# Optimization experiments

Measured on AMD Instinct MI355X. Metric: run time of the kernel, lower is better.

The kernel has to match this reference:

```python
import jax, jax.numpy as jnp
import numpy as np

N0, N1, N2 = 200000, 100000, 50000
DEG = 16
E0, E1 = N1 * DEG, N2 * DEG
EP = 500000
IN, H, EDGE_IN, MLP_H, NCLS = 64, 128, 16, 128, 8
EPS = 1e-5  # BatchNorm eps


def setup_inputs() -> dict:
    key = jax.random.key(0)
    ks = jax.random.split(key, 22)
    def w(k, shape, fan_in):
        return jax.random.normal(k, shape, dtype=jnp.float32) * (1.0 / np.sqrt(fan_in))
    inp = {
        'x_nodes': jax.random.normal(ks[0], (N0, IN), dtype=jnp.float32),
        'src0': jax.random.randint(ks[1], (E0,), 0, N0, dtype=jnp.int32),
        'dst0': jax.random.randint(ks[2], (E0,), 0, N1, dtype=jnp.int32),
        'src1': jax.random.randint(ks[3], (E1,), 0, N1, dtype=jnp.int32),
        'dst1': jax.random.randint(ks[4], (E1,), 0, N2, dtype=jnp.int32),
        'u': jax.random.randint(ks[5], (EP,), 0, N2, dtype=jnp.int32),
        'v': jax.random.randint(ks[6], (EP,), 0, N2, dtype=jnp.int32),
        'e_feat': jax.random.normal(ks[7], (EP, EDGE_IN), dtype=jnp.float32),
        # SAGEConv layer 0 (DGL mean aggregator: fc_self(h_dst) + fc_neigh(mean_neigh) + bias)
        'Ws0': w(ks[8], (IN, H), IN), 'Wn0': w(ks[9], (IN, H), IN), 'b0': jnp.zeros((H,), jnp.float32),
        'g0': jnp.ones((H,), jnp.float32), 'be0': jnp.zeros((H,), jnp.float32),
        # SAGEConv layer 1
        'Ws1': w(ks[10], (H, H), H), 'Wn1': w(ks[11], (H, H), H), 'b1': jnp.zeros((H,), jnp.float32),
        'g1': jnp.ones((H,), jnp.float32), 'be1': jnp.zeros((H,), jnp.float32),
        # edge MLP: Linear(2H+edge_in, MLP_H) -> ReLU -> (Dropout eval=no-op) -> Linear(MLP_H, NCLS)
        'W1': w(ks[12], (2 * H + EDGE_IN, MLP_H), 2 * H + EDGE_IN), 'bm1': jnp.zeros((MLP_H,), jnp.float32),
        'W2': w(ks[13], (MLP_H, NCLS), MLP_H), 'bm2': jnp.zeros((NCLS,), jnp.float32),
    }
    return inp


def _sage_mean(h_src, src, dst, num_dst, Ws, Wn, b):
    # gather neighbor feats, segment-mean over dst, then linear combine
    msgs = h_src[src]                                            # [E, d]
    agg = jax.ops.segment_sum(msgs, dst, num_segments=num_dst)   # [num_dst, d]
    deg = jax.ops.segment_sum(jnp.ones((src.shape[0],), h_src.dtype), dst, num_segments=num_dst)
    mean = agg / jnp.maximum(deg, 1.0)[:, None]
    h_dst = h_src[:num_dst]
    return h_dst @ Ws + mean @ Wn + b


def _bn_relu(x, gamma, beta):
    # training-mode BatchNorm1d over rows, followed by ReLU
    mu = x.mean(axis=0)
    var = x.var(axis=0)
    return jax.nn.relu(gamma * (x - mu) * jax.lax.rsqrt(var + EPS) + beta)


def reference(x_nodes, src0, dst0, src1, dst1, u, v, e_feat,
              Ws0, Wn0, b0, g0, be0, Ws1, Wn1, b1, g1, be1, W1, bm1, W2, bm2):
    h = _bn_relu(_sage_mean(x_nodes, src0, dst0, N1, Ws0, Wn0, b0), g0, be0)  # [N1, H]
    h = _bn_relu(_sage_mean(h, src1, dst1, N2, Ws1, Wn1, b1), g1, be1)        # [N2, H]
    e_repr = jnp.concatenate([h[u], h[v], e_feat], axis=1)                    # [EP, 2H+edge_in]
    hidden = jax.nn.relu(e_repr @ W1 + bm1)
    return hidden @ W2 + bm2                                                  # [EP, NCLS]
```

## Files before the change

### kernel.cpp

```cpp
#include <hip/hip_runtime.h>
#include <hip/hip_bf16.h>

#define CN0 200000
#define CN1 100000
#define CN2 50000
#define CE0 1600000
#define CE1 800000
#define CEP 500000
#define CIN 64
#define CH  128
#define CEIN 16
#define CMH 128
#define CNCLS 8

typedef __bf16 bf16x8 __attribute__((ext_vector_type(8)));
typedef float  f32x4  __attribute__((ext_vector_type(4)));
typedef unsigned short u16x8 __attribute__((ext_vector_type(8)));
typedef unsigned short u16x4 __attribute__((ext_vector_type(4)));

__device__ inline float b2f(unsigned short u) {
  union { unsigned int i; float f; } x; x.i = ((unsigned int)u) << 16; return x.f;
}
__device__ inline unsigned short f2bu(float f) {
  __hip_bfloat16 h = __float2bfloat16(f);
  return *reinterpret_cast<unsigned short*>(&h);
}

__global__ void k_hist(const int* __restrict__ dst, int n, int* __restrict__ cnt) {
  int i = blockIdx.x * blockDim.x + threadIdx.x;
  if (i < n) atomicAdd(&cnt[dst[i]], 1);
}

__global__ __launch_bounds__(256) void k_scan1(const int* __restrict__ cnt, int n,
                                               int* __restrict__ excl, int* __restrict__ bsum) {
  __shared__ int sh[256];
  int t = threadIdx.x;
  int base = blockIdx.x * 1024 + t * 4;
  int v[4];
#pragma unroll
  for (int i = 0; i < 4; i++) v[i] = (base + i < n) ? cnt[base + i] : 0;
  int tsum = v[0] + v[1] + v[2] + v[3];
  sh[t] = tsum; __syncthreads();
  for (int ofs = 1; ofs < 256; ofs <<= 1) {
    int x = (t >= ofs) ? sh[t - ofs] : 0; __syncthreads();
    sh[t] += x; __syncthreads();
  }
  int run = sh[t] - tsum;
  if (t == 255) bsum[blockIdx.x] = sh[255];
#pragma unroll
  for (int i = 0; i < 4; i++) {
    if (base + i < n) excl[base + i] = run;
    run += v[i];
  }
}

__global__ __launch_bounds__(256) void k_scan2(int* __restrict__ bsum, int n) {
  __shared__ int sh[256];
  int t = threadIdx.x;
  int v = (t < n) ? bsum[t] : 0;
  sh[t] = v; __syncthreads();
  for (int ofs = 1; ofs < 256; ofs <<= 1) {
    int x = (t >= ofs) ? sh[t - ofs] : 0; __syncthreads();
    sh[t] += x; __syncthreads();
  }
  if (t < n) bsum[t] = sh[t] - v;
}

__global__ void k_scan3(int* __restrict__ off, int* __restrict__ cur,
                        const int* __restrict__ bsum, int n, int total) {
  int i = blockIdx.x * blockDim.x + threadIdx.x;
  if (i < n) {
    int vv = off[i] + bsum[i >> 10];
    off[i] = vv; cur[i] = vv;
  }
  if (i == n) off[n] = total;
}

__global__ void k_reorder(const int* __restrict__ src, const int* __restrict__ dst,
                          int n, int* __restrict__ cur, int* __restrict__ srcs) {
  int i = blockIdx.x * blockDim.x + threadIdx.x;
  if (i < n) {
    int p = atomicAdd(&cur[dst[i]], 1);
    srcs[p] = src[i];
  }
}

__global__ __launch_bounds__(256) void k_gather64b(
    const __hip_bfloat16* __restrict__ xb, const int* __restrict__ off,
    const int* __restrict__ srcs, __hip_bfloat16* __restrict__ meanb, int nnodes) {
  int node = blockIdx.x * 4 + (threadIdx.x >> 6);
  if (node >= nnodes) return;
  int lane = threadIdx.x & 63;
  int g = lane >> 3;
  int f8 = (lane & 7) * 8;
  int s = off[node], e = off[node + 1];
  float acc[8] = {0.f,0.f,0.f,0.f,0.f,0.f,0.f,0.f};
  for (int p = s + g; p < e; p += 8) {
    int sn = srcs[p];
    u16x8 v = *reinterpret_cast<const u16x8*>(xb + (long long)sn * CIN + f8);
#pragma unroll
    for (int j = 0; j < 8; j++) acc[j] += b2f(v[j]);
  }
#pragma unroll
  for (int m = 8; m < 64; m <<= 1)
#pragma unroll
    for (int j = 0; j < 8; j++) acc[j] += __shfl_xor(acc[j], m, 64);
  if (g == 0) {
    float inv = 1.0f / (float)max(e - s, 1);
    u16x8 o;
#pragma unroll
    for (int j = 0; j < 8; j++) o[j] = f2bu(acc[j] * inv);
    *reinterpret_cast<u16x8*>(meanb + (long long)node * CIN + f8) = o;
  }
}

__global__ __launch_bounds__(256) void k_gather128b(
    const __hip_bfloat16* __restrict__ hb, const int* __restrict__ off,
    const int* __restrict__ srcs, __hip_bfloat16* __restrict__ meanb, int nnodes) {
  int node = blockIdx.x * 4 + (threadIdx.x >> 6);
  if (node >= nnodes) return;
  int lane = threadIdx.x & 63;
  int g = lane >> 4;
  int f8 = (lane & 15) * 8;
  int s = off[node], e = off[node + 1];
  float acc[8] = {0.f,0.f,0.f,0.f,0.f,0.f,0.f,0.f};
  for (int p = s + g; p < e; p += 4) {
    int sn = srcs[p];
    u16x8 v = *reinterpret_cast<const u16x8*>(hb + (long long)sn * CH + f8);
#pragma unroll
    for (int j = 0; j < 8; j++) acc[j] += b2f(v[j]);
  }
#pragma unroll
  for (int m = 16; m < 64; m <<= 1)
#pragma unroll
    for (int j = 0; j < 8; j++) acc[j] += __shfl_xor(acc[j], m, 64);
  if (g == 0) {
    float inv = 1.0f / (float)max(e - s, 1);
    u16x8 o;
#pragma unroll
    for (int j = 0; j < 8; j++) o[j] = f2bu(acc[j] * inv);
    *reinterpret_cast<u16x8*>(meanb + (long long)node * CH + f8) = o;
  }
}

template<int KA>
__global__ __launch_bounds__(256) void k_sage_mfma(
    const __hip_bfloat16* __restrict__ A1, const __hip_bfloat16* __restrict__ A2,
    const __hip_bfloat16* __restrict__ wT, const float* __restrict__ bias,
    __hip_bfloat16* __restrict__ outb, float* __restrict__ stats, int M) {
  __shared__ float ssum[CH], ssq[CH];
  int tid = threadIdx.x;
  int lane = tid & 63;
  int w = tid >> 6;
  int wm = w & 1, wn = w >> 1;
  int l15 = lane & 15, lk = lane >> 4;
  int r0 = blockIdx.x * 64;

  if (tid < CH) { ssum[tid] = 0.f; ssq[tid] = 0.f; }

  int rA = r0 + wm * 32 + l15;
  int rB = rA + 16;
  int rAc = min(rA, M - 1), rBc = min(rB, M - 1);
  const __hip_bfloat16* a1A = A1 + (long long)rAc * KA + lk * 8;
  const __hip_bfloat16* a1B = A1 + (long long)rBc * KA + lk * 8;
  const __hip_bfloat16* a2A = A2 + (long long)rAc * KA + lk * 8;
  const __hip_bfloat16* a2B = A2 + (long long)rBc * KA + lk * 8;
  const __hip_bfloat16* wp[4];
#pragma unroll
  for (int nf = 0; nf < 4; nf++)
    wp[nf] = wT + (long long)(wn * 64 + nf * 16 + l15) * (2 * KA) + lk * 8;

  f32x4 acc[2][4];
#pragma unroll
  for (int nf = 0; nf < 4; nf++) {
    float bv = bias[wn * 64 + nf * 16 + l15];
#pragma unroll
    for (int m = 0; m < 2; m++) {
      acc[m][nf][0] = bv; acc[m][nf][1] = bv;
      acc[m][nf][2] = bv; acc[m][nf][3] = bv;
    }
  }

  constexpr int HS = KA / 32;
#pragma unroll
  for (int kk = 0; kk < 2 * HS; kk++) {
    bf16x8 a0, a1v;
    if (kk < HS) {
      a0  = *reinterpret_cast<const bf16x8*>(a1A + kk * 32);
      a1v = *reinterpret_cast<const bf16x8*>(a1B + kk * 32);
    } else {
      a0  = *reinterpret_cast<const bf16x8*>(a2A + (kk - HS) * 32);
      a1v = *reinterpret_cast<const bf16x8*>(a2B + (kk - HS) * 32);
    }
#pragma unroll
    for (int nf = 0; nf < 4; nf++) {
      bf16x8 b = *reinterpret_cast<const bf16x8*>(wp[nf] + kk * 32);
      acc[0][nf] = __builtin_amdgcn_mfma_f32_16x16x32_bf16(a0,  b, acc[0][nf], 0, 0, 0);
      acc[1][nf] = __builtin_amdgcn_mfma_f32_16x16x32_bf16(a1v, b, acc[1][nf], 0, 0, 0);
    }
  }
  __syncthreads();

  unsigned short* ob = reinterpret_cast<unsigned short*>(outb);
#pragma unroll
  for (int nf = 0; nf < 4; nf++) {
    float cs = 0.f, cq = 0.f;
#pragma unroll
    for (int m = 0; m < 2; m++)
#pragma unroll
      for (int r = 0; r < 4; r++) {
        int row = r0 + wm * 32 + m * 16 + lk * 4 + r;
        if (row < M) {
          float v = acc[m][nf][r];
          cs += v; cq = fmaf(v, v, cq);
          ob[(long long)row * CH + wn * 64 + nf * 16 + l15] = f2bu(v);
        }
      }
    cs += __shfl_xor(cs, 16, 64); cq += __shfl_xor(cq, 16, 64);
    cs += __shfl_xor(cs, 32, 64); cq += __shfl_xor(cq, 32, 64);
    if (lk == 0) {
      atomicAdd(&ssum[wn * 64 + nf * 16 + l15], cs);
      atomicAdd(&ssq [wn * 64 + nf * 16 + l15], cq);
    }
  }
  __syncthreads();
  if (tid < CH) {
    atomicAdd(&stats[tid], ssum[tid]);
    atomicAdd(&stats[CH + tid], ssq[tid]);
  }
}

__global__ void k_bnrelu_b(__hip_bfloat16* __restrict__ h, int nrows,
                           const float* __restrict__ stats,
                           const float* __restrict__ g, const float* __restrict__ be) {
  int total8 = nrows * (CH / 8);
  float inv_n = 1.0f / (float)nrows;
  for (int i = blockIdx.x * blockDim.x + threadIdx.x; i < total8;
       i += gridDim.x * blockDim.x) {
    int cg = (i & 15) * 8;
    u16x8 v = reinterpret_cast<u16x8*>(h)[i];
    u16x8 o;
#pragma unroll
    for (int j = 0; j < 8; j++) {
      int c = cg + j;
      float mu = stats[c] * inv_n;
      float var = stats[CH + c] * inv_n - mu * mu;
      float rs = rsqrtf(var + 1e-5f);
      float val = (b2f(v[j]) - mu) * rs * g[c] + be[c];
      o[j] = f2bu(fmaxf(val, 0.0f));
    }
    reinterpret_cast<u16x8*>(h)[i] = o;
  }
}

__global__ void k_f2b4(const float* __restrict__ src, __hip_bfloat16* __restrict__ dst, int n4) {
  for (int i = blockIdx.x * blockDim.x + threadIdx.x; i < n4; i += gridDim.x * blockDim.x) {
    float4 v = reinterpret_cast<const float4*>(src)[i];
    u16x4 o; o[0] = f2bu(v.x); o[1] = f2bu(v.y); o[2] = f2bu(v.z); o[3] = f2bu(v.w);
    reinterpret_cast<u16x4*>(dst)[i] = o;
  }
}

__global__ void k_prep(const float* __restrict__ Ws0, const float* __restrict__ Wn0,
                       const float* __restrict__ Ws1, const float* __restrict__ Wn1,
                       const float* __restrict__ W1, const float* __restrict__ W2,
                       __hip_bfloat16* __restrict__ wT0, __hip_bfloat16* __restrict__ wT1,
                       __hip_bfloat16* __restrict__ w1t, __hip_bfloat16* __restrict__ w2t) {
  int t = blockIdx.x * blockDim.x + threadIdx.x;
  if (t < 16384) {
    int n = t >> 7, k = t & 127;
    wT0[t] = __float2bfloat16(k < 64 ? Ws0[k * CH + n] : Wn0[(k - 64) * CH + n]);
    return;
  }
  t -= 16384;
  if (t < 32768) {
    int n = t >> 8, k = t & 255;
    wT1[t] = __float2bfloat16(k < 128 ? Ws1[k * CH + n] : Wn1[(k - 128) * CH + n]);
    return;
  }
  t -= 32768;
  if (t < 34816) {
    int n = t / 272, k = t % 272;
    w1t[t] = __float2bfloat16(W1[k * CMH + n]);
    return;
  }
  t -= 34816;
  if (t < 2048) {
    int c = t >> 7, k = t & 127;
    w2t[t] = __float2bfloat16(c < CNCLS ? W2[k * CNCLS + c] : 0.0f);
  }
}

__global__ __launch_bounds__(256) void k_edge_mfma(
    const __hip_bfloat16* __restrict__ h2b, const int* __restrict__ u,
    const int* __restrict__ v, const float* __restrict__ ef,
    const __hip_bfloat16* __restrict__ w1t, const float* __restrict__ bm1,
    const __hip_bfloat16* __restrict__ w2t, const float* __restrict__ bm2,
    float* __restrict__ out) {
  __shared__ __align__(16) unsigned short hid[64][152];
  int tid = threadIdx.x;
  int lane = tid & 63;
  int w = tid >> 6;
  int wm = w & 1;
  int wn = w >> 1;
  int l15 = lane & 15, lk = lane >> 4;
  int e0 = blockIdx.x * 64;

  int eA = e0 + wm * 32 + l15;
  int eB = eA + 16;
  int eAc = min(eA, CEP - 1), eBc = min(eB, CEP - 1);
  int uA = u[eAc], uB = u[eBc], vA = v[eAc], vB = v[eBc];

  const __hip_bfloat16* auP = h2b + (long long)uA * CH + lk * 8;
  const __hip_bfloat16* buP = h2b + (long long)uB * CH + lk * 8;
  const __hip_bfloat16* avP = h2b + (long long)vA * CH + lk * 8;
  const __hip_bfloat16* bvP = h2b + (long long)vB * CH + lk * 8;

  const __hip_bfloat16* wb[4];
#pragma unroll
  for (int nf = 0; nf < 4; nf++)
    wb[nf] = w1t + (long long)(wn * 64 + nf * 16 + l15) * (2 * CH + CEIN) + lk * 8;

  bf16x8 zf = {};
  bf16x8 aefA = zf, aefB = zf;
  if (lk < 2) {
    const float* pA = ef + (long long)eAc * CEIN + lk * 8;
    const float* pB = ef + (long long)eBc * CEIN + lk * 8;
    float4 a0 = *reinterpret_cast<const float4*>(pA);
    float4 a1 = *reinterpret_cast<const float4*>(pA + 4);
    float4 b0 = *reinterpret_cast<const float4*>(pB);
    float4 b1 = *reinterpret_cast<const float4*>(pB + 4);
    u16x8 ua, ub;
    ua[0]=f2bu(a0.x); ua[1]=f2bu(a0.y); ua[2]=f2bu(a0.z); ua[3]=f2bu(a0.w);
    ua[4]=f2bu(a1.x); ua[5]=f2bu(a1.y); ua[6]=f2bu(a1.z); ua[7]=f2bu(a1.w);
    ub[0]=f2bu(b0.x); ub[1]=f2bu(b0.y); ub[2]=f2bu(b0.z); ub[3]=f2bu(b0.w);
    ub[4]=f2bu(b1.x); ub[5]=f2bu(b1.y); ub[6]=f2bu(b1.z); ub[7]=f2bu(b1.w);
    aefA = *reinterpret_cast<bf16x8*>(&ua);
    aefB = *reinterpret_cast<bf16x8*>(&ub);
  }

  f32x4 acc[2][4];
#pragma unroll
  for (int nf = 0; nf < 4; nf++) {
    float bias = bm1[wn * 64 + nf * 16 + l15];
#pragma unroll
    for (int m = 0; m < 2; m++) {
      acc[m][nf][0] = bias; acc[m][nf][1] = bias;
      acc[m][nf][2] = bias; acc[m][nf][3] = bias;
    }
  }

#pragma unroll
  for (int kk = 0; kk < 9; kk++) {
    bf16x8 a0, a1;
    if (kk < 4) {
      a0 = *reinterpret_cast<const bf16x8*>(auP + kk * 32);
      a1 = *reinterpret_cast<const bf16x8*>(buP + kk * 32);
    } else if (kk < 8) {
      a0 = *reinterpret_cast<const bf16x8*>(avP + (kk - 4) * 32);
      a1 = *reinterpret_cast<const bf16x8*>(bvP + (kk - 4) * 32);
    } else {
      a0 = aefA;
      a1 = aefB;
    }
#pragma unroll
    for (int nf = 0; nf < 4; nf++) {
      bf16x8 b;
      if (kk < 8) b = *reinterpret_cast<const bf16x8*>(wb[nf] + kk * 32);
      else        b = (lk < 2) ? *reinterpret_cast<const bf16x8*>(wb[nf] + 256) : zf;
      acc[0][nf] = __builtin_amdgcn_mfma_f32_16x16x32_bf16(a0, b, acc[0][nf], 0, 0, 0);
      acc[1][nf] = __builtin_amdgcn_mfma_f32_16x16x32_bf16(a1, b, acc[1][nf], 0, 0, 0);
    }
  }

#pragma unroll
  for (int m = 0; m < 2; m++)
#pragma unroll
    for (int nf = 0; nf < 4; nf++)
#pragma unroll
      for (int r = 0; r < 4; r++) {
        int row = wm * 32 + m * 16 + lk * 4 + r;
        int col = wn * 64 + nf * 16 + l15;
        hid[row][col] = f2bu(fmaxf(acc[m][nf][r], 0.0f));
      }
  __syncthreads();

  {
    int we = w * 16;
    const __hip_bfloat16* w2p = w2t + (long long)l15 * CMH + lk * 8;
    float bv2 = (l15 < CNCLS) ? bm2[l15] : 0.0f;
    f32x4 o; o[0] = bv2; o[1] = bv2; o[2] = bv2; o[3] = bv2;
#pragma unroll
    for (int kk = 0; kk < 4; kk++) {
      bf16x8 a = *reinterpret_cast<const bf16x8*>(
          reinterpret_cast<const unsigned short*>(&hid[we + l15][0]) + kk * 32 + lk * 8);
      bf16x8 b = *reinterpret_cast<const bf16x8*>(w2p + kk * 32);
      o = __builtin_amdgcn_mfma_f32_16x16x32_bf16(a, b, o, 0, 0, 0);
    }
    if (l15 < CNCLS) {
#pragma unroll
      for (int r = 0; r < 4; r++) {
        int e = e0 + we + lk * 4 + r;
        if (e < CEP) out[(long long)e * CNCLS + l15] = o[r];
      }
    }
  }
}

extern "C" void kernel_launch(void* const* d_in, const int* in_sizes, int n_in,
                              void* d_out, int out_size, void* d_ws, size_t ws_size,
                              hipStream_t stream) {
  const float* x_nodes = (const float*)d_in[0];
  const int*   src0    = (const int*)d_in[1];
  const int*   dst0    = (const int*)d_in[2];
  const int*   src1    = (const int*)d_in[3];
  const int*   dst1    = (const int*)d_in[4];
  const int*   u       = (const int*)d_in[5];
  const int*   v       = (const int*)d_in[6];
  const float* e_feat  = (const float*)d_in[7];
  const float* Ws0     = (const float*)d_in[8];
  const float* Wn0     = (const float*)d_in[9];
  const float* b0      = (const float*)d_in[10];
  const float* g0      = (const float*)d_in[11];
  const float* be0     = (const float*)d_in[12];
  const float* Ws1     = (const float*)d_in[13];
  const float* Wn1     = (const float*)d_in[14];
  const float* b1      = (const float*)d_in[15];
  const float* g1      = (const float*)d_in[16];
  const float* be1     = (const float*)d_in[17];
  const float* W1      = (const float*)d_in[18];
  const float* bm1     = (const float*)d_in[19];
  const float* W2      = (const float*)d_in[20];
  const float* bm2     = (const float*)d_in[21];
  float* out = (float*)d_out;

  float* ws = (float*)d_ws;
  __hip_bfloat16* xb    = (__hip_bfloat16*)(ws + 0);
  __hip_bfloat16* h2b   = (__hip_bfloat16*)(ws + 0);
  __hip_bfloat16* meanb = (__hip_bfloat16*)(ws + 6400000);
  __hip_bfloat16* h1b   = (__hip_bfloat16*)(ws + 9600000);
  __hip_bfloat16* wT0   = (__hip_bfloat16*)(ws + 16000000);
  __hip_bfloat16* wT1   = (__hip_bfloat16*)(ws + 16010000);
  __hip_bfloat16* w1tb  = (__hip_bfloat16*)(ws + 16030000);
  __hip_bfloat16* w2tb  = (__hip_bfloat16*)(ws + 16048000);
  float* s0   = ws + 16050000;
  float* s1   = ws + 16050256;
  int*   offA = (int*)(ws + 16060000);
  int*   curA = (int*)(ws + 16170000);
  int*   cntA = (int*)(ws + 16280000);
  int*   bsum = (int*)(ws + 16390000);
  int*   srcs = (int*)(ws + 16400000);

  hipMemsetAsync(s0, 0, 512 * sizeof(float), stream);
  k_prep<<<(16384 + 32768 + 34816 + 2048 + 255) / 256, 256, 0, stream>>>(
      Ws0, Wn0, Ws1, Wn1, W1, W2, wT0, wT1, w1tb, w2tb);
  k_f2b4<<<2048, 256, 0, stream>>>(x_nodes, xb, CN0 * CIN / 4);

  hipMemsetAsync(cntA, 0, CN1 * sizeof(int), stream);
  k_hist<<<(CE0 + 255) / 256, 256, 0, stream>>>(dst0, CE0, cntA);
  {
    int nblk = (CN1 + 1023) / 1024;
    k_scan1<<<nblk, 256, 0, stream>>>(cntA, CN1, offA, bsum);
    k_scan2<<<1, 256, 0, stream>>>(bsum, nblk);
    k_scan3<<<(CN1 + 256) / 256, 256, 0, stream>>>(offA, curA, bsum, CN1, CE0);
  }
  k_reorder<<<(CE0 + 255) / 256, 256, 0, stream>>>(src0, dst0, CE0, curA, srcs);

  k_gather64b<<<(CN1 + 3) / 4, 256, 0, stream>>>(xb, offA, srcs, meanb, CN1);
  k_sage_mfma<CIN><<<(CN1 + 63) / 64, 256, 0, stream>>>(xb, meanb, wT0, b0, h1b, s0, CN1);
  k_bnrelu_b<<<2048, 256, 0, stream>>>(h1b, CN1, s0, g0, be0);

  hipMemsetAsync(cntA, 0, CN2 * sizeof(int), stream);
  k_hist<<<(CE1 + 255) / 256, 256, 0, stream>>>(dst1, CE1, cntA);
  {
    int nblk = (CN2 + 1023) / 1024;
    k_scan1<<<nblk, 256, 0, stream>>>(cntA, CN2, offA, bsum);
    k_scan2<<<1, 256, 0, stream>>>(bsum, nblk);
    k_scan3<<<(CN2 + 256) / 256, 256, 0, stream>>>(offA, curA, bsum, CN2, CE1);
  }
  k_reorder<<<(CE1 + 255) / 256, 256, 0, stream>>>(src1, dst1, CE1, curA, srcs);

  k_gather128b<<<(CN2 + 3) / 4, 256, 0, stream>>>(h1b, offA, srcs, meanb, CN2);
  k_sage_mfma<CH><<<(CN2 + 63) / 64, 256, 0, stream>>>(h1b, meanb, wT1, b1, h2b, s1, CN2);
  k_bnrelu_b<<<2048, 256, 0, stream>>>(h2b, CN2, s1, g1, be1);

  k_edge_mfma<<<(CEP + 63) / 64, 256, 0, stream>>>(h2b, u, v, e_feat, w1tb, bm1, w2tb, bm2, out);
}
```

Before: 781.7 us.

## Precompute per-node W1 projections and merge both layers' CSR builds

The first edge-MLP layer is split algebraically: each of the 50k nodes is projected through the u-half and v-half of W1 once (k_pgemm into a bf16 table). Each edge then gathers two 128-wide projected rows and adds a small edge-feature MFMA, instead of running a K=272 GEMM per edge. Separately, the histogram, scan and reorder for both graph layers are merged into single launches over concatenated offsets, and the memsets are folded into k_prep. This cuts per-edge MFMA work and launch count, at the cost of an extra node-level GEMM, a 25.6MB intermediate, and bf16 rounding of the projections before summation.

```diff
diff --git a/kernel.cpp b/kernel.cpp
--- a/kernel.cpp
+++ b/kernel.cpp
@@ -12,6 +12,8 @@
 #define CEIN 16
 #define CMH 128
 #define CNCLS 8
+#define NTOT (CN1 + CN2)
+#define ETOT (CE0 + CE1)
 
 typedef __bf16 bf16x8 __attribute__((ext_vector_type(8)));
 typedef float  f32x4  __attribute__((ext_vector_type(4)));
@@ -26,9 +28,60 @@
   return *reinterpret_cast<unsigned short*>(&h);
 }
 
-__global__ void k_hist(const int* __restrict__ dst, int n, int* __restrict__ cnt) {
+__global__ void k_prep(const float* __restrict__ Ws0, const float* __restrict__ Wn0,
+                       const float* __restrict__ Ws1, const float* __restrict__ Wn1,
+                       const float* __restrict__ W1, const float* __restrict__ W2,
+                       __hip_bfloat16* __restrict__ wT0, __hip_bfloat16* __restrict__ wT1,
+                       __hip_bfloat16* __restrict__ wab, __hip_bfloat16* __restrict__ w1cT,
+                       __hip_bfloat16* __restrict__ w2t,
+                       int* __restrict__ cnt, float* __restrict__ stats) {
+  int t0 = blockIdx.x * blockDim.x + threadIdx.x;
+  if (t0 < NTOT + 1) cnt[t0] = 0;
+  if (t0 < 512) stats[t0] = 0.f;
+  int t = t0;
+  if (t < 16384) {
+    int n = t >> 7, k = t & 127;
+    wT0[t] = __float2bfloat16(k < 64 ? Ws0[k * CH + n] : Wn0[(k - 64) * CH + n]);
+    return;
+  }
+  t -= 16384;
+  if (t < 32768) {
+    int n = t >> 8, k = t & 255;
+    wT1[t] = __float2bfloat16(k < 128 ? Ws1[k * CH + n] : Wn1[(k - 128) * CH + n]);
+    return;
+  }
+  t -= 32768;
+  if (t < 32768) {
+    int n = t >> 7, k = t & 127;
+    wab[t] = __float2bfloat16(n < 128 ? W1[k * CMH + n] : W1[(128 + k) * CMH + (n - 128)]);
+    return;
+  }
+  t -= 32768;
+  if (t < 4096) {
+    int n = t >> 5, k = t & 31;
+    w1cT[t] = __float2bfloat16(k < CEIN ? W1[(256 + k) * CMH + n] : 0.0f);
+    return;
+  }
+  t -= 4096;
+  if (t < 2048) {
+    int col = t >> 7, k = t & 127;
+    w2t[t] = __float2bfloat16(col < CNCLS ? W2[k * CNCLS + col] : 0.0f);
+  }
+}
+
+__global__ void k_f2b4(const float* __restrict__ src, __hip_bfloat16* __restrict__ dst, int n4) {
+  for (int i = blockIdx.x * blockDim.x + threadIdx.x; i < n4; i += gridDim.x * blockDim.x) {
+    float4 v = reinterpret_cast<const float4*>(src)[i];
+    u16x4 o; o[0] = f2bu(v.x); o[1] = f2bu(v.y); o[2] = f2bu(v.z); o[3] = f2bu(v.w);
+    reinterpret_cast<u16x4*>(dst)[i] = o;
+  }
+}
+
+__global__ void k_hist2(const int* __restrict__ dst0, const int* __restrict__ dst1,
+                        int* __restrict__ cnt) {
   int i = blockIdx.x * blockDim.x + threadIdx.x;
-  if (i < n) atomicAdd(&cnt[dst[i]], 1);
+  if (i < CE0) atomicAdd(&cnt[dst0[i]], 1);
+  else if (i < ETOT) atomicAdd(&cnt[CN1 + dst1[i - CE0]], 1);
 }
 
 __global__ __launch_bounds__(256) void k_scan1(const int* __restrict__ cnt, int n,
@@ -54,34 +107,37 @@
   }
 }
 
-__global__ __launch_bounds__(256) void k_scan2(int* __restrict__ bsum, int n) {
+__global__ __launch_bounds__(256) void k_scan23(int* __restrict__ off, int* __restrict__ cur,
+                                                const int* __restrict__ bsum, int nblk,
+                                                int n, int total) {
   __shared__ int sh[256];
   int t = threadIdx.x;
-  int v = (t < n) ? bsum[t] : 0;
+  int v = (t < nblk) ? bsum[t] : 0;
   sh[t] = v; __syncthreads();
   for (int ofs = 1; ofs < 256; ofs <<= 1) {
     int x = (t >= ofs) ? sh[t - ofs] : 0; __syncthreads();
     sh[t] += x; __syncthreads();
   }
-  if (t < n) bsum[t] = sh[t] - v;
-}
-
-__global__ void k_scan3(int* __restrict__ off, int* __restrict__ cur,
-                        const int* __restrict__ bsum, int n, int total) {
+  int i = blockIdx.x * 256 + t;
+  if (i < n) {
+    int grp = i >> 10;
+    int add = grp ? sh[grp - 1] : 0;
+    int vv = off[i] + add;
+    off[i] = vv; cur[i] = vv;
+  }
+  if (i == n) off[n] = total;
+}
+
+__global__ void k_reorder2(const int* __restrict__ src0, const int* __restrict__ dst0,
+                           const int* __restrict__ src1, const int* __restrict__ dst1,
+                           int* __restrict__ cur, int* __restrict__ srcs) {
   int i = blockIdx.x * blockDim.x + threadIdx.x;
-  if (i < n) {
-    int vv = off[i] + bsum[i >> 10];
-    off[i] = vv; cur[i] = vv;
-  }
-  if (i == n) off[n] = total;
-}
-
-__global__ void k_reorder(const int* __restrict__ src, const int* __restrict__ dst,
-                          int n, int* __restrict__ cur, int* __restrict__ srcs) {
-  int i = blockIdx.x * blockDim.x + threadIdx.x;
-  if (i < n) {
-    int p = atomicAdd(&cur[dst[i]], 1);
-    srcs[p] = src[i];
+  if (i < CE0) {
+    int p = atomicAdd(&cur[dst0[i]], 1);
+    srcs[p] = src0[i];
+  } else if (i < ETOT) {
+    int p = atomicAdd(&cur[CN1 + dst1[i - CE0]], 1);
+    srcs[p] = src1[i - CE0];
   }
 }
 
@@ -253,136 +309,116 @@
   }
 }
 
-__global__ void k_f2b4(const float* __restrict__ src, __hip_bfloat16* __restrict__ dst, int n4) {
-  for (int i = blockIdx.x * blockDim.x + threadIdx.x; i < n4; i += gridDim.x * blockDim.x) {
-    float4 v = reinterpret_cast<const float4*>(src)[i];
-    u16x4 o; o[0] = f2bu(v.x); o[1] = f2bu(v.y); o[2] = f2bu(v.z); o[3] = f2bu(v.w);
-    reinterpret_cast<u16x4*>(dst)[i] = o;
-  }
-}
-
-__global__ void k_prep(const float* __restrict__ Ws0, const float* __restrict__ Wn0,
-                       const float* __restrict__ Ws1, const float* __restrict__ Wn1,
-                       const float* __restrict__ W1, const float* __restrict__ W2,
-                       __hip_bfloat16* __restrict__ wT0, __hip_bfloat16* __restrict__ wT1,
-                       __hip_bfloat16* __restrict__ w1t, __hip_bfloat16* __restrict__ w2t) {
-  int t = blockIdx.x * blockDim.x + threadIdx.x;
-  if (t < 16384) {
-    int n = t >> 7, k = t & 127;
-    wT0[t] = __float2bfloat16(k < 64 ? Ws0[k * CH + n] : Wn0[(k - 64) * CH + n]);
-    return;
-  }
-  t -= 16384;
-  if (t < 32768) {
-    int n = t >> 8, k = t & 255;
-    wT1[t] = __float2bfloat16(k < 128 ? Ws1[k * CH + n] : Wn1[(k - 128) * CH + n]);
-    return;
-  }
-  t -= 32768;
-  if (t < 34816) {
-    int n = t / 272, k = t % 272;
-    w1t[t] = __float2bfloat16(W1[k * CMH + n]);
-    return;
-  }
-  t -= 34816;
-  if (t < 2048) {
-    int c = t >> 7, k = t & 127;
-    w2t[t] = __float2bfloat16(c < CNCLS ? W2[k * CNCLS + c] : 0.0f);
-  }
-}
-
-__global__ __launch_bounds__(256) void k_edge_mfma(
-    const __hip_bfloat16* __restrict__ h2b, const int* __restrict__ u,
+__global__ __launch_bounds__(256) void k_pgemm(
+    const __hip_bfloat16* __restrict__ h2b, const __hip_bfloat16* __restrict__ wab,
+    __hip_bfloat16* __restrict__ paP, int M) {
+  int tid = threadIdx.x, lane = tid & 63, w = tid >> 6;
+  int wm = w & 1, wn = w >> 1;
+  int l15 = lane & 15, lk = lane >> 4;
+  int r0 = blockIdx.x * 64;
+  int rA = r0 + wm * 32 + l15, rB = rA + 16;
+  int rAc = min(rA, M - 1), rBc = min(rB, M - 1);
+  const __hip_bfloat16* aA = h2b + (long long)rAc * CH + lk * 8;
+  const __hip_bfloat16* aB = h2b + (long long)rBc * CH + lk * 8;
+  const __hip_bfloat16* wp[8];
+#pragma unroll
+  for (int nf = 0; nf < 8; nf++)
+    wp[nf] = wab + (long long)(wn * 128 + nf * 16 + l15) * CH + lk * 8;
+
+  f32x4 acc[2][8];
+#pragma unroll
+  for (int m = 0; m < 2; m++)
+#pragma unroll
+    for (int nf = 0; nf < 8; nf++) {
+      acc[m][nf][0] = 0.f; acc[m][nf][1] = 0.f; acc[m][nf][2] = 0.f; acc[m][nf][3] = 0.f;
+    }
+
+#pragma unroll
+  for (int kk = 0; kk < 4; kk++) {
+    bf16x8 a0 = *reinterpret_cast<const bf16x8*>(aA + kk * 32);
+    bf16x8 a1 = *reinterpret_cast<const bf16x8*>(aB + kk * 32);
+#pragma unroll
+    for (int nf = 0; nf < 8; nf++) {
+      bf16x8 b = *reinterpret_cast<const bf16x8*>(wp[nf] + kk * 32);
+      acc[0][nf] = __builtin_amdgcn_mfma_f32_16x16x32_bf16(a0, b, acc[0][nf], 0, 0, 0);
+      acc[1][nf] = __builtin_amdgcn_mfma_f32_16x16x32_bf16(a1, b, acc[1][nf], 0, 0, 0);
+    }
+  }
+
+  unsigned short* ob = reinterpret_cast<unsigned short*>(paP);
+#pragma unroll
+  for (int m = 0; m < 2; m++)
+#pragma unroll
+    for (int nf = 0; nf < 8; nf++)
+#pragma unroll
+      for (int r = 0; r < 4; r++) {
+        int row = r0 + wm * 32 + m * 16 + lk * 4 + r;
+        if (row < M)
+          ob[(long long)row * 256 + wn * 128 + nf * 16 + l15] = f2bu(acc[m][nf][r]);
+      }
+}
+
+__global__ __launch_bounds__(256) void k_edge_v3(
+    const __hip_bfloat16* __restrict__ paP, const int* __restrict__ u,
     const int* __restrict__ v, const float* __restrict__ ef,
-    const __hip_bfloat16* __restrict__ w1t, const float* __restrict__ bm1,
+    const __hip_bfloat16* __restrict__ w1cT, const float* __restrict__ bm1,
     const __hip_bfloat16* __restrict__ w2t, const float* __restrict__ bm2,
     float* __restrict__ out) {
   __shared__ __align__(16) unsigned short hid[64][152];
-  int tid = threadIdx.x;
-  int lane = tid & 63;
-  int w = tid >> 6;
-  int wm = w & 1;
-  int wn = w >> 1;
+  int tid = threadIdx.x, lane = tid & 63, w = tid >> 6;
   int l15 = lane & 15, lk = lane >> 4;
   int e0 = blockIdx.x * 64;
 
-  int eA = e0 + wm * 32 + l15;
-  int eB = eA + 16;
-  int eAc = min(eA, CEP - 1), eBc = min(eB, CEP - 1);
-  int uA = u[eAc], uB = u[eBc], vA = v[eAc], vB = v[eBc];
-
-  const __hip_bfloat16* auP = h2b + (long long)uA * CH + lk * 8;
-  const __hip_bfloat16* buP = h2b + (long long)uB * CH + lk * 8;
-  const __hip_bfloat16* avP = h2b + (long long)vA * CH + lk * 8;
-  const __hip_bfloat16* bvP = h2b + (long long)vB * CH + lk * 8;
-
-  const __hip_bfloat16* wb[4];
-#pragma unroll
-  for (int nf = 0; nf < 4; nf++)
-    wb[nf] = w1t + (long long)(wn * 64 + nf * 16 + l15) * (2 * CH + CEIN) + lk * 8;
-
-  bf16x8 zf = {};
-  bf16x8 aefA = zf, aefB = zf;
-  if (lk < 2) {
-    const float* pA = ef + (long long)eAc * CEIN + lk * 8;
-    const float* pB = ef + (long long)eBc * CEIN + lk * 8;
-    float4 a0 = *reinterpret_cast<const float4*>(pA);
-    float4 a1 = *reinterpret_cast<const float4*>(pA + 4);
-    float4 b0 = *reinterpret_cast<const float4*>(pB);
-    float4 b1 = *reinterpret_cast<const float4*>(pB + 4);
-    u16x8 ua, ub;
-    ua[0]=f2bu(a0.x); ua[1]=f2bu(a0.y); ua[2]=f2bu(a0.z); ua[3]=f2bu(a0.w);
-    ua[4]=f2bu(a1.x); ua[5]=f2bu(a1.y); ua[6]=f2bu(a1.z); ua[7]=f2bu(a1.w);
-    ub[0]=f2bu(b0.x); ub[1]=f2bu(b0.y); ub[2]=f2bu(b0.z); ub[3]=f2bu(b0.w);
-    ub[4]=f2bu(b1.x); ub[5]=f2bu(b1.y); ub[6]=f2bu(b1.z); ub[7]=f2bu(b1.w);
-    aefA = *reinterpret_cast<bf16x8*>(&ua);
-    aefB = *reinterpret_cast<bf16x8*>(&ub);
-  }
-
-  f32x4 acc[2][4];
-#pragma unroll
-  for (int nf = 0; nf < 4; nf++) {
-    float bias = bm1[wn * 64 + nf * 16 + l15];
-#pragma unroll
-    for (int m = 0; m < 2; m++) {
-      acc[m][nf][0] = bias; acc[m][nf][1] = bias;
-      acc[m][nf][2] = bias; acc[m][nf][3] = bias;
-    }
-  }
-
-#pragma unroll
-  for (int kk = 0; kk < 9; kk++) {
-    bf16x8 a0, a1;
-    if (kk < 4) {
-      a0 = *reinterpret_cast<const bf16x8*>(auP + kk * 32);
-      a1 = *reinterpret_cast<const bf16x8*>(buP + kk * 32);
-    } else if (kk < 8) {
-      a0 = *reinterpret_cast<const bf16x8*>(avP + (kk - 4) * 32);
-      a1 = *reinterpret_cast<const bf16x8*>(bvP + (kk - 4) * 32);
-    } else {
-      a0 = aefA;
-      a1 = aefB;
-    }
-#pragma unroll
-    for (int nf = 0; nf < 4; nf++) {
-      bf16x8 b;
-      if (kk < 8) b = *reinterpret_cast<const bf16x8*>(wb[nf] + kk * 32);
-      else        b = (lk < 2) ? *reinterpret_cast<const bf16x8*>(wb[nf] + 256) : zf;
-      acc[0][nf] = __builtin_amdgcn_mfma_f32_16x16x32_bf16(a0, b, acc[0][nf], 0, 0, 0);
-      acc[1][nf] = __builtin_amdgcn_mfma_f32_16x16x32_bf16(a1, b, acc[1][nf], 0, 0, 0);
-    }
-  }
-
-#pragma unroll
-  for (int m = 0; m < 2; m++)
-#pragma unroll
-    for (int nf = 0; nf < 4; nf++)
-#pragma unroll
-      for (int r = 0; r < 4; r++) {
-        int row = wm * 32 + m * 16 + lk * 4 + r;
-        int col = wn * 64 + nf * 16 + l15;
-        hid[row][col] = f2bu(fmaxf(acc[m][nf][r], 0.0f));
-      }
+  {
+    int ec = min(e0 + w * 16 + l15, CEP - 1);
+    bf16x8 a = {};
+    if (lk < 2) {
+      const float* p = ef + (long long)ec * CEIN + lk * 8;
+      float4 x0 = *reinterpret_cast<const float4*>(p);
+      float4 x1 = *reinterpret_cast<const float4*>(p + 4);
+      u16x8 t;
+      t[0]=f2bu(x0.x); t[1]=f2bu(x0.y); t[2]=f2bu(x0.z); t[3]=f2bu(x0.w);
+      t[4]=f2bu(x1.x); t[5]=f2bu(x1.y); t[6]=f2bu(x1.z); t[7]=f2bu(x1.w);
+      a = *reinterpret_cast<bf16x8*>(&t);
+    }
+#pragma unroll
+    for (int nf = 0; nf < 8; nf++) {
+      f32x4 acc;
+      float bv = bm1[nf * 16 + l15];
+      acc[0] = bv; acc[1] = bv; acc[2] = bv; acc[3] = bv;
+      bf16x8 b = *reinterpret_cast<const bf16x8*>(w1cT + (nf * 16 + l15) * 32 + lk * 8);
+      acc = __builtin_amdgcn_mfma_f32_16x16x32_bf16(a, b, acc, 0, 0, 0);
+#pragma unroll
+      for (int r = 0; r < 4; r++)
+        hid[w * 16 + lk * 4 + r][nf * 16 + l15] = f2bu(acc[r]);
+    }
+  }
+  __syncthreads();
+
+  {
+    int e = tid >> 2, q = tid & 3;
+    int ec = min(e0 + e, CEP - 1);
+    int ue = u[ec], ve = v[ec];
+    const unsigned short* pa = reinterpret_cast<const unsigned short*>(paP)
+                               + (long long)ue * 256 + q * 32;
+    const unsigned short* pb = reinterpret_cast<const unsigned short*>(paP)
+                               + (long long)ve * 256 + 128 + q * 32;
+    u16x8 ra[4], rb[4], rh[4];
+#pragma unroll
+    for (int i = 0; i < 4; i++) {
+      ra[i] = *reinterpret_cast<const u16x8*>(pa + i * 8);
+      rb[i] = *reinterpret_cast<const u16x8*>(pb + i * 8);
+      rh[i] = *reinterpret_cast<const u16x8*>(&hid[e][q * 32 + i * 8]);
+    }
+#pragma unroll
+    for (int i = 0; i < 4; i++) {
+      u16x8 o;
+#pragma unroll
+      for (int j = 0; j < 8; j++)
+        o[j] = f2bu(fmaxf(b2f(rh[i][j]) + b2f(ra[i][j]) + b2f(rb[i][j]), 0.0f));
+      *reinterpret_cast<u16x8*>(&hid[e][q * 32 + i * 8]) = o;
+    }
+  }
   __syncthreads();
 
   {
@@ -439,50 +475,41 @@
   __hip_bfloat16* h2b   = (__hip_bfloat16*)(ws + 0);
   __hip_bfloat16* meanb = (__hip_bfloat16*)(ws + 6400000);
   __hip_bfloat16* h1b   = (__hip_bfloat16*)(ws + 9600000);
-  __hip_bfloat16* wT0   = (__hip_bfloat16*)(ws + 16000000);
-  __hip_bfloat16* wT1   = (__hip_bfloat16*)(ws + 16010000);
-  __hip_bfloat16* w1tb  = (__hip_bfloat16*)(ws + 16030000);
-  __hip_bfloat16* w2tb  = (__hip_bfloat16*)(ws + 16048000);
-  float* s0   = ws + 16050000;
-  float* s1   = ws + 16050256;
-  int*   offA = (int*)(ws + 16060000);
-  int*   curA = (int*)(ws + 16170000);
-  int*   cntA = (int*)(ws + 16280000);
-  int*   bsum = (int*)(ws + 16390000);
-  int*   srcs = (int*)(ws + 16400000);
-
-  hipMemsetAsync(s0, 0, 512 * sizeof(float), stream);
-  k_prep<<<(16384 + 32768 + 34816 + 2048 + 255) / 256, 256, 0, stream>>>(
-      Ws0, Wn0, Ws1, Wn1, W1, W2, wT0, wT1, w1tb, w2tb);
+  __hip_bfloat16* paP   = (__hip_bfloat16*)(ws + 16000000);
+  __hip_bfloat16* wT0   = (__hip_bfloat16*)(ws + 22400000);
+  __hip_bfloat16* wT1   = (__hip_bfloat16*)(ws + 22410000);
+  __hip_bfloat16* wab   = (__hip_bfloat16*)(ws + 22430000);
+  __hip_bfloat16* w1cT  = (__hip_bfloat16*)(ws + 22450000);
+  __hip_bfloat16* w2t   = (__hip_bfloat16*)(ws + 22453000);
+  float* stats = ws + 22455000;
+  float* s0 = stats;
+  float* s1 = stats + 256;
+  int*   off  = (int*)(ws + 22456000);
+  int*   cur  = (int*)(ws + 22610000);
+  int*   cnt  = (int*)(ws + 22770000);
+  int*   bsum = (int*)(ws + 22930000);
+  int*   srcs = (int*)(ws + 22931000);
+
+  k_prep<<<(NTOT + 256) / 256, 256, 0, stream>>>(
+      Ws0, Wn0, Ws1, Wn1, W1, W2, wT0, wT1, wab, w1cT, w2t, cnt, stats);
   k_f2b4<<<2048, 256, 0, stream>>>(x_nodes, xb, CN0 * CIN / 4);
 
-  hipMemsetAsync(cntA, 0, CN1 * sizeof(int), stream);
-  k_hist<<<(CE0 + 255) / 256, 256, 0, stream>>>(dst0, CE0, cntA);
+  k_hist2<<<(ETOT + 255) / 256, 256, 0, stream>>>(dst0, dst1, cnt);
   {
-    int nblk = (CN1 + 1023) / 1024;
-    k_scan1<<<nblk, 256, 0, stream>>>(cntA, CN1, offA, bsum);
-    k_scan2<<<1, 256, 0, stream>>>(bsum, nblk);
-    k_scan3<<<(CN1 + 256) / 256, 256, 0, stream>>>(offA, curA, bsum, CN1, CE0);
-  }
-  k_reorder<<<(CE0 + 255) / 256, 256, 0, stream>>>(src0, dst0, CE0, curA, srcs);
-
-  k_gather64b<<<(CN1 + 3) / 4, 256, 0, stream>>>(xb, offA, srcs, meanb, CN1);
+    int nblk = (NTOT + 1023) / 1024;
+    k_scan1<<<nblk, 256, 0, stream>>>(cnt, NTOT, off, bsum);
+    k_scan23<<<(NTOT + 256) / 256, 256, 0, stream>>>(off, cur, bsum, nblk, NTOT, ETOT);
+  }
+  k_reorder2<<<(ETOT + 255) / 256, 256, 0, stream>>>(src0, dst0, src1, dst1, cur, srcs);
+
+  k_gather64b<<<(CN1 + 3) / 4, 256, 0, stream>>>(xb, off, srcs, meanb, CN1);
   k_sage_mfma<CIN><<<(CN1 + 63) / 64, 256, 0, stream>>>(xb, meanb, wT0, b0, h1b, s0, CN1);
   k_bnrelu_b<<<2048, 256, 0, stream>>>(h1b, CN1, s0, g0, be0);
 
-  hipMemsetAsync(cntA, 0, CN2 * sizeof(int), stream);
-  k_hist<<<(CE1 + 255) / 256, 256, 0, stream>>>(dst1, CE1, cntA);
-  {
-    int nblk = (CN2 + 1023) / 1024;
-    k_scan1<<<nblk, 256, 0, stream>>>(cntA, CN2, offA, bsum);
-    k_scan2<<<1, 256, 0, stream>>>(bsum, nblk);
-    k_scan3<<<(CN2 + 256) / 256, 256, 0, stream>>>(offA, curA, bsum, CN2, CE1);
-  }
-  k_reorder<<<(CE1 + 255) / 256, 256, 0, stream>>>(src1, dst1, CE1, curA, srcs);
-
-  k_gather128b<<<(CN2 + 3) / 4, 256, 0, stream>>>(h1b, offA, srcs, meanb, CN2);
+  k_gather128b<<<(CN2 + 3) / 4, 256, 0, stream>>>(h1b, off + CN1, srcs, meanb, CN2);
   k_sage_mfma<CH><<<(CN2 + 63) / 64, 256, 0, stream>>>(h1b, meanb, wT1, b1, h2b, s1, CN2);
-  k_bnrelu_b<<<2048, 256, 0, stream>>>(h2b, CN2, s1, g1, be1);
-
-  k_edge_mfma<<<(CEP + 63) / 64, 256, 0, stream>>>(h2b, u, v, e_feat, w1tb, bm1, w2tb, bm2, out);
-}
+  k_bnrelu_b<<<1024, 256, 0, stream>>>(h2b, CN2, s1, g1, be1);
+
+  k_pgemm<<<(CN2 + 63) / 64, 256, 0, stream>>>(h2b, wab, paP, CN2);
+  k_edge_v3<<<(CEP + 63) / 64, 256, 0, stream>>>(paP, u, v, e_feat, w1cT, bm1, w2t, bm2, out);
+}
```

Measured after the change: 772.6 us. No clear change (-1.2%).
